# Performance work log

Hardware: AMD Instinct MI355X
Metric: run time of the kernel (lower is better)

The kernel has to match this reference:

```python
import jax, jax.numpy as jnp
import numpy as np

B, T, D = 2, 2048, 1024
H, HD = 16, 64  # num_heads, key_size

def setup_inputs() -> dict:
    key = jax.random.key(0)
    ks = jax.random.split(key, 5)
    s = 1.0 / np.sqrt(D)  # VarianceScaling(1.0, fan_in) approx
    return {
        "query": jax.random.normal(ks[0], (B, T, D), dtype=jnp.float32),
        "wq": jax.random.normal(ks[1], (D, H * HD), dtype=jnp.float32) * s,
        "bq": jnp.zeros((H * HD,), dtype=jnp.float32),
        "wk": jax.random.normal(ks[2], (D, H * HD), dtype=jnp.float32) * s,
        "bk": jnp.zeros((H * HD,), dtype=jnp.float32),
        "wv": jax.random.normal(ks[3], (D, H * HD), dtype=jnp.float32) * s,
        "bv": jnp.zeros((H * HD,), dtype=jnp.float32),
        "wo": jax.random.normal(ks[4], (H * HD, D), dtype=jnp.float32) * (1.0 / np.sqrt(H * HD)),
        "bo": jnp.zeros((D,), dtype=jnp.float32),
    }

def reference(query, wq, bq, wk, bk, wv, bv, wo, bo):
    b, t, _ = query.shape
    proj = lambda w, bias: (query @ w + bias).reshape(b, t, H, HD)
    q = proj(wq, bq) / np.sqrt(HD).astype(np.float32)  # fixed scaling on queries
    k = proj(wk, bk)
    v = proj(wv, bv)
    logits = jnp.einsum('bthd,bThd->bhtT', q, k)  # [B,H,T,T]
    causal = jnp.tril(jnp.ones((t, t), dtype=logits.dtype))
    logits = logits - 1e10 * (1.0 - causal)
    weights = jax.nn.softmax(logits, axis=-1)
    attn = jnp.einsum('bhtT,bThd->bthd', weights, v)
    attn_vec = attn.reshape(b, t, H * HD)
    return attn_vec @ wo + bo
```

## Files before the change

kernel.cpp:

```cpp
#include <hip/hip_runtime.h>
#include <hip/hip_bf16.h>
#include <stdint.h>
#include <math.h>

typedef short bf16x8 __attribute__((ext_vector_type(8)));
typedef float f32x4 __attribute__((ext_vector_type(4)));
typedef __hip_bfloat16 bf16;

#define MFMA16(a, b, c) __builtin_amdgcn_mfma_f32_16x16x32_bf16((a), (b), (c), 0, 0, 0)

__device__ __forceinline__ void glds16(const void* g, void* l) {
  __builtin_amdgcn_global_load_lds((const __attribute__((address_space(1))) void*)g,
                                   (__attribute__((address_space(3))) void*)l, 16, 0, 0);
}

__device__ __forceinline__ bf16x8 ld8(const bf16* p) {
  return *reinterpret_cast<const bf16x8*>(p);
}


__global__ void k_cvt_x(const float* __restrict__ x, bf16* __restrict__ o, int n4) {
  int i = blockIdx.x * blockDim.x + threadIdx.x;
  if (i < n4) {
    float4 v = reinterpret_cast<const float4*>(x)[i];
    bf16 a0 = __float2bfloat16(v.x), a1 = __float2bfloat16(v.y);
    bf16 a2 = __float2bfloat16(v.z), a3 = __float2bfloat16(v.w);
    ushort4 r;
    r.x = reinterpret_cast<unsigned short&>(a0);
    r.y = reinterpret_cast<unsigned short&>(a1);
    r.z = reinterpret_cast<unsigned short&>(a2);
    r.w = reinterpret_cast<unsigned short&>(a3);
    reinterpret_cast<ushort4*>(o)[i] = r;
  }
}

__global__ void k_transpose_cvt(const float* __restrict__ wq, const float* __restrict__ wk,
                                const float* __restrict__ wv, const float* __restrict__ wo,
                                bf16* __restrict__ Wqkvt, bf16* __restrict__ Wot) {
  __shared__ float tile[32][33];
  const int z = blockIdx.z;
  const float* src = (z == 0) ? wq : (z == 1) ? wk : (z == 2) ? wv : wo;
  bf16* dst = (z < 3) ? (Wqkvt + (size_t)z * 1024 * 1024) : Wot;
  const int tx = threadIdx.x & 31, ty = threadIdx.x >> 5;
  const int x = blockIdx.x * 32 + tx;
  const int y0 = blockIdx.y * 32;
#pragma unroll
  for (int i = 0; i < 4; ++i) tile[ty + i * 8][tx] = src[(size_t)(y0 + ty + i * 8) * 1024 + x];
  __syncthreads();
#pragma unroll
  for (int i = 0; i < 4; ++i) {
    int c = blockIdx.x * 32 + ty + i * 8;
    dst[(size_t)c * 1024 + y0 + tx] = __float2bfloat16(tile[tx][ty + i * 8]);
  }
}


__device__ __forceinline__ void gemm_core(const bf16* __restrict__ A, const bf16* __restrict__ Bt,
                                          int K, int arow0, int bcol0,
                                          bf16* As, bf16* Bs, f32x4 acc[4][4]) {
  const int tid = threadIdx.x, lane = tid & 63, w = tid >> 6;
  const int rsub = lane >> 3, slot = lane & 7;
  const int srcslot = slot ^ rsub;
  const int wrow = (w >> 1) * 64, wcol = (w & 1) * 64;
  const int lr = lane & 15, lg = lane >> 4;
  const int nkt = K >> 6;
  for (int kt = 0; kt < nkt; ++kt) {
    const int k0 = kt * 64;
    if (kt) __syncthreads();
#pragma unroll
    for (int i = 0; i < 4; ++i) {
      const int chunk = w * 4 + i;
      glds16(A + (size_t)(arow0 + chunk * 8 + rsub) * K + k0 + srcslot * 8, As + chunk * 512);
      glds16(Bt + (size_t)(bcol0 + chunk * 8 + rsub) * K + k0 + srcslot * 8, Bs + chunk * 512);
    }
    __syncthreads();
#pragma unroll
    for (int kk = 0; kk < 2; ++kk) {
      bf16x8 af[4], bfv[4];
#pragma unroll
      for (int m = 0; m < 4; ++m) {
        const int row = wrow + m * 16 + lr;
        const int byte = (row * 128 + ((kk * 32 + lg * 8) << 1)) ^ ((row & 7) << 4);
        af[m] = *reinterpret_cast<const bf16x8*>(reinterpret_cast<const char*>(As) + byte);
      }
#pragma unroll
      for (int n = 0; n < 4; ++n) {
        const int row = wcol + n * 16 + lr;
        const int byte = (row * 128 + ((kk * 32 + lg * 8) << 1)) ^ ((row & 7) << 4);
        bfv[n] = *reinterpret_cast<const bf16x8*>(reinterpret_cast<const char*>(Bs) + byte);
      }
#pragma unroll
      for (int m = 0; m < 4; ++m)
#pragma unroll
        for (int n = 0; n < 4; ++n) acc[m][n] = MFMA16(af[m], bfv[n], acc[m][n]);
    }
  }
}


__global__ __launch_bounds__(256) void k_gemm_qkv(
    const bf16* __restrict__ X, const bf16* __restrict__ Wt,
    const float* __restrict__ bq, const float* __restrict__ bk, const float* __restrict__ bv,
    bf16* __restrict__ Qo, bf16* __restrict__ Ko, bf16* __restrict__ Vt) {
  __shared__ bf16 As[128 * 64], Bs[128 * 64];
  f32x4 acc[4][4];
#pragma unroll
  for (int i = 0; i < 4; ++i)
#pragma unroll
    for (int j = 0; j < 4; ++j) acc[i][j] = (f32x4){0.f, 0.f, 0.f, 0.f};
  const int arow0 = blockIdx.y * 128, bcol0 = blockIdx.x * 128;
  gemm_core(X, Wt, 1024, arow0, bcol0, As, Bs, acc);
  const int lane = threadIdx.x & 63, w = threadIdx.x >> 6;
  const int wrow = (w >> 1) * 64, wcol = (w & 1) * 64;
  const int lr = lane & 15, lg = lane >> 4;
#pragma unroll
  for (int mi = 0; mi < 4; ++mi) {
#pragma unroll
    for (int ni = 0; ni < 4; ++ni) {
      const int r0 = arow0 + wrow + mi * 16 + lg * 4;
      const int col = bcol0 + wcol + ni * 16 + lr;
      const int which = col >> 10, cw = col & 1023, h = cw >> 6, hd = cw & 63;
      const int b = r0 >> 11, t0 = r0 & 2047;
      if (which == 2) {
        const float bias = bv[cw];
        ushort4 pk;
#pragma unroll
        for (int j = 0; j < 4; ++j) {
          bf16 hv = __float2bfloat16(acc[mi][ni][j] + bias);
          reinterpret_cast<unsigned short*>(&pk)[j] = reinterpret_cast<unsigned short&>(hv);
        }
        *reinterpret_cast<ushort4*>(Vt + ((size_t)((b * 16 + h) * 64 + hd)) * 2048 + t0) = pk;
      } else {
        const float bias = which ? bk[cw] : bq[cw];
        const float scale = which ? 1.0f : 0.125f;
        bf16* dst = which ? Ko : Qo;
#pragma unroll
        for (int j = 0; j < 4; ++j) {
          float v = (acc[mi][ni][j] + bias) * scale;
          dst[((size_t)((b * 16 + h) * 2048) + t0 + j) * 64 + hd] = __float2bfloat16(v);
        }
      }
    }
  }
}


__global__ __launch_bounds__(256) void k_attn(const bf16* __restrict__ Q, const bf16* __restrict__ Kc,
                                              const bf16* __restrict__ Vt, bf16* __restrict__ attn) {
  __shared__ bf16 Ks[2][64 * 64];
  __shared__ bf16 Vs[2][64 * 64];
  __shared__ bf16 Plds[4][16 * 64];
  const int lane = threadIdx.x & 63, w = threadIdx.x >> 6;
  const int lr = lane & 15, lg = lane >> 4;
  const int rsub = lane >> 3, slot = lane & 7;
  const int srcslot = slot ^ rsub;
  const int bh = blockIdx.x;
  const int qt = 31 - blockIdx.y;
  const int b = bh >> 4, h = bh & 15;
  const bf16* Qp = Q + (size_t)bh * 2048 * 64;
  const bf16* Kp = Kc + (size_t)bh * 2048 * 64;
  const bf16* Vp = Vt + (size_t)bh * 64 * 2048;

  const int q0 = qt * 64 + w * 16;
  const bf16x8 qa0 = ld8(Qp + (size_t)(q0 + lr) * 64 + lg * 8);
  const bf16x8 qa1 = ld8(Qp + (size_t)(q0 + lr) * 64 + 32 + lg * 8);
  f32x4 o[4];
#pragma unroll
  for (int n = 0; n < 4; ++n) o[n] = (f32x4){0.f, 0.f, 0.f, 0.f};
  float l_[4] = {0.f, 0.f, 0.f, 0.f};
  const int nkv = qt + 1;
  const float LOG2E = 1.4426950408889634f;
  const float MBIAS = -8.0f * LOG2E;

#pragma unroll
  for (int i = 0; i < 2; ++i) {
    const int ck = w * 2 + i;
    glds16(Kp + (size_t)(ck * 8 + rsub) * 64 + srcslot * 8, &Ks[0][ck * 512]);
    glds16(Vp + (size_t)(ck * 8 + rsub) * 2048 + srcslot * 8, &Vs[0][ck * 512]);
  }
  __syncthreads();
  int cur = 0;

#pragma unroll 1
  for (int it = 0; it < nkv; ++it) {
    const int kv0 = it * 64;
    if (it + 1 < nkv) {
#pragma unroll
      for (int i = 0; i < 2; ++i) {
        const int ck = w * 2 + i;
        glds16(Kp + (size_t)((it + 1) * 64 + ck * 8 + rsub) * 64 + srcslot * 8, &Ks[cur ^ 1][ck * 512]);
        glds16(Vp + (size_t)(ck * 8 + rsub) * 2048 + (it + 1) * 64 + srcslot * 8, &Vs[cur ^ 1][ck * 512]);
      }
    }
    f32x4 s[4];
    const char* Kb = reinterpret_cast<const char*>(&Ks[cur][0]);
#pragma unroll
    for (int n = 0; n < 4; ++n) {
      const int row = n * 16 + lr;
      const int rsw = (row & 7) << 4;
      bf16x8 kb0 = *reinterpret_cast<const bf16x8*>(Kb + ((row * 128 + lg * 16) ^ rsw));
      bf16x8 kb1 = *reinterpret_cast<const bf16x8*>(Kb + ((row * 128 + 64 + lg * 16) ^ rsw));
      f32x4 zz = {0.f, 0.f, 0.f, 0.f};
      s[n] = MFMA16(qa0, kb0, zz);
      s[n] = MFMA16(qa1, kb1, s[n]);
    }
    if (it == nkv - 1) {
#pragma unroll
      for (int n = 0; n < 4; ++n)
#pragma unroll
        for (int j = 0; j < 4; ++j)
          if (kv0 + n * 16 + lr > q0 + lg * 4 + j) s[n][j] = -1e30f;
    }
    float p[4][4];
#pragma unroll
    for (int n = 0; n < 4; ++n)
#pragma unroll
      for (int j = 0; j < 4; ++j) {
        p[n][j] = exp2f(fmaf(s[n][j], LOG2E, MBIAS));
        l_[j] += p[n][j];
      }
#pragma unroll
    for (int n = 0; n < 4; ++n)
#pragma unroll
      for (int j = 0; j < 4; ++j) {
        const int row = lg * 4 + j, col = n * 16 + lr;
        Plds[w][row * 64 + (col ^ ((row & 7) << 3))] = __float2bfloat16(p[n][j]);
      }
    bf16x8 pa[2];
#pragma unroll
    for (int kc = 0; kc < 2; ++kc) {
      const int byte = (lr * 128 + ((kc * 32 + lg * 8) << 1)) ^ ((lr & 7) << 4);
      pa[kc] = *reinterpret_cast<const bf16x8*>(reinterpret_cast<const char*>(&Plds[w][0]) + byte);
    }
    const char* Vb = reinterpret_cast<const char*>(&Vs[cur][0]);
#pragma unroll
    for (int n2 = 0; n2 < 4; ++n2) {
#pragma unroll
      for (int kc = 0; kc < 2; ++kc) {
        const int row = n2 * 16 + lr;
        const int rsw = (row & 7) << 4;
        bf16x8 vb = *reinterpret_cast<const bf16x8*>(Vb + ((row * 128 + (kc * 32 + lg * 8) * 2) ^ rsw));
        o[n2] = MFMA16(pa[kc], vb, o[n2]);
      }
    }
    __syncthreads();
    cur ^= 1;
  }
#pragma unroll
  for (int j = 0; j < 4; ++j) {
    float v = l_[j];
#pragma unroll
    for (int off = 1; off < 16; off <<= 1) v += __shfl_xor(v, off);
    l_[j] = v;
  }
#pragma unroll
  for (int j = 0; j < 4; ++j) {
    const float inv = 1.0f / l_[j];
    const int qq = q0 + lg * 4 + j;
#pragma unroll
    for (int n2 = 0; n2 < 4; ++n2)
      attn[((size_t)(b * 2048 + qq)) * 1024 + h * 64 + n2 * 16 + lr] = __float2bfloat16(o[n2][j] * inv);
  }
}


__global__ __launch_bounds__(256) void k_gemm_out(const bf16* __restrict__ A, const bf16* __restrict__ Wot,
                                                  const float* __restrict__ bo, float* __restrict__ out) {
  __shared__ bf16 As[128 * 64], Bs[128 * 64];
  f32x4 acc[4][4];
#pragma unroll
  for (int i = 0; i < 4; ++i)
#pragma unroll
    for (int j = 0; j < 4; ++j) acc[i][j] = (f32x4){0.f, 0.f, 0.f, 0.f};
  const int arow0 = blockIdx.y * 128, bcol0 = blockIdx.x * 128;
  gemm_core(A, Wot, 1024, arow0, bcol0, As, Bs, acc);
  const int lane = threadIdx.x & 63, w = threadIdx.x >> 6;
  const int wrow = (w >> 1) * 64, wcol = (w & 1) * 64;
  const int lr = lane & 15, lg = lane >> 4;
#pragma unroll
  for (int mi = 0; mi < 4; ++mi) {
#pragma unroll
    for (int ni = 0; ni < 4; ++ni) {
      const int r0 = arow0 + wrow + mi * 16 + lg * 4;
      const int col = bcol0 + wcol + ni * 16 + lr;
      const float bias = bo[col];
#pragma unroll
      for (int j = 0; j < 4; ++j) out[(size_t)(r0 + j) * 1024 + col] = acc[mi][ni][j] + bias;
    }
  }
}


extern "C" void kernel_launch(void* const* d_in, const int* in_sizes, int n_in,
                              void* d_out, int out_size, void* d_ws, size_t ws_size,
                              hipStream_t stream) {
  const float* query = (const float*)d_in[0];
  const float* wq = (const float*)d_in[1];
  const float* bq = (const float*)d_in[2];
  const float* wk = (const float*)d_in[3];
  const float* bk = (const float*)d_in[4];
  const float* wv = (const float*)d_in[5];
  const float* bv = (const float*)d_in[6];
  const float* wo = (const float*)d_in[7];
  const float* bo = (const float*)d_in[8];
  float* out = (float*)d_out;
  char* ws = (char*)d_ws;
  const size_t MB = 1u << 20;
  bf16* X     = (bf16*)(ws + 0);
  bf16* Wqkvt = (bf16*)(ws + 8 * MB);
  bf16* Wot   = (bf16*)(ws + 14 * MB);
  bf16* Qb    = (bf16*)(ws + 16 * MB);
  bf16* Kb    = (bf16*)(ws + 24 * MB);
  bf16* Vt    = (bf16*)(ws + 32 * MB);
  bf16* attn  = (bf16*)(ws + 40 * MB);

  k_cvt_x<<<4096, 256, 0, stream>>>(query, X, 4096 * 1024 / 4);
  k_transpose_cvt<<<dim3(32, 32, 4), 256, 0, stream>>>(wq, wk, wv, wo, Wqkvt, Wot);
  k_gemm_qkv<<<dim3(24, 32), 256, 0, stream>>>(X, Wqkvt, bq, bk, bv, Qb, Kb, Vt);
  k_attn<<<dim3(32, 32), 256, 0, stream>>>(Qb, Kb, Vt, attn);
  k_gemm_out<<<dim3(8, 32), 256, 0, stream>>>(attn, Wot, bo, out);
}
```

Before: 112.8 us.

## Double attention query tile to 128 rows and fold log2e scaling into Q

The attention kernel now handles 128 query rows per block (32 per wave, as two 16-row subtiles), so each K/V tile staged in LDS and loaded into registers serves twice as many queries, and the grid is halved. The log2e factor is folded into the Q projection scale, and the constant softmax bias is folded into the MFMA accumulator init, which removes an FMA per logit. P is converted to bf16 by truncation instead of rounding. The costs are more register pressure from the extra accumulators and K/V fragments, fewer blocks to fill the device, and some warp divergence on the causal diagonal.

```diff
diff --git a/kernel.cpp b/kernel.cpp
--- a/kernel.cpp
+++ b/kernel.cpp
@@ -113,6 +113,7 @@
   const int lane = threadIdx.x & 63, w = threadIdx.x >> 6;
   const int wrow = (w >> 1) * 64, wcol = (w & 1) * 64;
   const int lr = lane & 15, lg = lane >> 4;
+  const float QSCALE = 0.125f * 1.4426950408889634f;
 #pragma unroll
   for (int mi = 0; mi < 4; ++mi) {
 #pragma unroll
@@ -132,7 +133,7 @@
         *reinterpret_cast<ushort4*>(Vt + ((size_t)((b * 16 + h) * 64 + hd)) * 2048 + t0) = pk;
       } else {
         const float bias = which ? bk[cw] : bq[cw];
-        const float scale = which ? 1.0f : 0.125f;
+        const float scale = which ? 1.0f : QSCALE;
         bf16* dst = which ? Ko : Qo;
 #pragma unroll
         for (int j = 0; j < 4; ++j) {
@@ -155,22 +156,28 @@
   const int rsub = lane >> 3, slot = lane & 7;
   const int srcslot = slot ^ rsub;
   const int bh = blockIdx.x;
-  const int qt = 31 - blockIdx.y;
+  const int qt = 15 - blockIdx.y;
   const int b = bh >> 4, h = bh & 15;
   const bf16* Qp = Q + (size_t)bh * 2048 * 64;
   const bf16* Kp = Kc + (size_t)bh * 2048 * 64;
   const bf16* Vp = Vt + (size_t)bh * 64 * 2048;
 
-  const int q0 = qt * 64 + w * 16;
-  const bf16x8 qa0 = ld8(Qp + (size_t)(q0 + lr) * 64 + lg * 8);
-  const bf16x8 qa1 = ld8(Qp + (size_t)(q0 + lr) * 64 + 32 + lg * 8);
-  f32x4 o[4];
-#pragma unroll
-  for (int n = 0; n < 4; ++n) o[n] = (f32x4){0.f, 0.f, 0.f, 0.f};
-  float l_[4] = {0.f, 0.f, 0.f, 0.f};
-  const int nkv = qt + 1;
-  const float LOG2E = 1.4426950408889634f;
-  const float MBIAS = -8.0f * LOG2E;
+  const int q0 = qt * 128 + w * 32;
+  bf16x8 qa[2][2];
+#pragma unroll
+  for (int m = 0; m < 2; ++m) {
+    qa[m][0] = ld8(Qp + (size_t)(q0 + m * 16 + lr) * 64 + lg * 8);
+    qa[m][1] = ld8(Qp + (size_t)(q0 + m * 16 + lr) * 64 + 32 + lg * 8);
+  }
+  f32x4 o[2][4];
+#pragma unroll
+  for (int m = 0; m < 2; ++m)
+#pragma unroll
+    for (int n = 0; n < 4; ++n) o[m][n] = (f32x4){0.f, 0.f, 0.f, 0.f};
+  float l_[2][4] = {{0.f, 0.f, 0.f, 0.f}, {0.f, 0.f, 0.f, 0.f}};
+  const int nkv = (qt + 1) * 2;
+  const float MBIAS = -8.0f * 1.4426950408889634f;
+  const f32x4 minit = {MBIAS, MBIAS, MBIAS, MBIAS};
 
 #pragma unroll
   for (int i = 0; i < 2; ++i) {
@@ -192,74 +199,82 @@
         glds16(Vp + (size_t)(ck * 8 + rsub) * 2048 + (it + 1) * 64 + srcslot * 8, &Vs[cur ^ 1][ck * 512]);
       }
     }
-    f32x4 s[4];
-    const char* Kb = reinterpret_cast<const char*>(&Ks[cur][0]);
-#pragma unroll
-    for (int n = 0; n < 4; ++n) {
-      const int row = n * 16 + lr;
-      const int rsw = (row & 7) << 4;
-      bf16x8 kb0 = *reinterpret_cast<const bf16x8*>(Kb + ((row * 128 + lg * 16) ^ rsw));
-      bf16x8 kb1 = *reinterpret_cast<const bf16x8*>(Kb + ((row * 128 + 64 + lg * 16) ^ rsw));
-      f32x4 zz = {0.f, 0.f, 0.f, 0.f};
-      s[n] = MFMA16(qa0, kb0, zz);
-      s[n] = MFMA16(qa1, kb1, s[n]);
-    }
-    if (it == nkv - 1) {
-#pragma unroll
-      for (int n = 0; n < 4; ++n)
-#pragma unroll
-        for (int j = 0; j < 4; ++j)
-          if (kv0 + n * 16 + lr > q0 + lg * 4 + j) s[n][j] = -1e30f;
-    }
-    float p[4][4];
-#pragma unroll
-    for (int n = 0; n < 4; ++n)
-#pragma unroll
-      for (int j = 0; j < 4; ++j) {
-        p[n][j] = exp2f(fmaf(s[n][j], LOG2E, MBIAS));
-        l_[j] += p[n][j];
-      }
-#pragma unroll
-    for (int n = 0; n < 4; ++n)
-#pragma unroll
-      for (int j = 0; j < 4; ++j) {
-        const int row = lg * 4 + j, col = n * 16 + lr;
-        Plds[w][row * 64 + (col ^ ((row & 7) << 3))] = __float2bfloat16(p[n][j]);
-      }
-    bf16x8 pa[2];
-#pragma unroll
-    for (int kc = 0; kc < 2; ++kc) {
-      const int byte = (lr * 128 + ((kc * 32 + lg * 8) << 1)) ^ ((lr & 7) << 4);
-      pa[kc] = *reinterpret_cast<const bf16x8*>(reinterpret_cast<const char*>(&Plds[w][0]) + byte);
-    }
-    const char* Vb = reinterpret_cast<const char*>(&Vs[cur][0]);
-#pragma unroll
-    for (int n2 = 0; n2 < 4; ++n2) {
-#pragma unroll
-      for (int kc = 0; kc < 2; ++kc) {
+    if (kv0 <= q0 + 31) {
+      bf16x8 kf0[4], kf1[4];
+      const char* Kb = reinterpret_cast<const char*>(&Ks[cur][0]);
+#pragma unroll
+      for (int n = 0; n < 4; ++n) {
+        const int row = n * 16 + lr;
+        const int rsw = (row & 7) << 4;
+        kf0[n] = *reinterpret_cast<const bf16x8*>(Kb + ((row * 128 + lg * 16) ^ rsw));
+        kf1[n] = *reinterpret_cast<const bf16x8*>(Kb + ((row * 128 + 64 + lg * 16) ^ rsw));
+      }
+      bf16x8 vf[4][2];
+      const char* Vb = reinterpret_cast<const char*>(&Vs[cur][0]);
+#pragma unroll
+      for (int n2 = 0; n2 < 4; ++n2) {
         const int row = n2 * 16 + lr;
         const int rsw = (row & 7) << 4;
-        bf16x8 vb = *reinterpret_cast<const bf16x8*>(Vb + ((row * 128 + (kc * 32 + lg * 8) * 2) ^ rsw));
-        o[n2] = MFMA16(pa[kc], vb, o[n2]);
+#pragma unroll
+        for (int kc = 0; kc < 2; ++kc)
+          vf[n2][kc] = *reinterpret_cast<const bf16x8*>(Vb + ((row * 128 + (kc * 32 + lg * 8) * 2) ^ rsw));
+      }
+#pragma unroll
+      for (int m = 0; m < 2; ++m) {
+        const int qm0 = q0 + m * 16;
+        if (kv0 > qm0 + 15) continue;
+        f32x4 s[4];
+#pragma unroll
+        for (int n = 0; n < 4; ++n) {
+          s[n] = MFMA16(qa[m][0], kf0[n], minit);
+          s[n] = MFMA16(qa[m][1], kf1[n], s[n]);
+        }
+        if (kv0 + 63 > qm0) {
+#pragma unroll
+          for (int n = 0; n < 4; ++n)
+#pragma unroll
+            for (int j = 0; j < 4; ++j)
+              if (kv0 + n * 16 + lr > qm0 + lg * 4 + j) s[n][j] = -1e30f;
+        }
+        unsigned short* Pw = reinterpret_cast<unsigned short*>(&Plds[w][0]);
+#pragma unroll
+        for (int n = 0; n < 4; ++n)
+#pragma unroll
+          for (int j = 0; j < 4; ++j) {
+            float p = exp2f(s[n][j]);
+            l_[m][j] += p;
+            const int row = lg * 4 + j, col = n * 16 + lr;
+            Pw[row * 64 + (col ^ ((row & 7) << 3))] = (unsigned short)(__float_as_uint(p) >> 16);
+          }
+        bf16x8 pa[2];
+#pragma unroll
+        for (int kc = 0; kc < 2; ++kc) {
+          const int byte = (lr * 128 + ((kc * 32 + lg * 8) << 1)) ^ ((lr & 7) << 4);
+          pa[kc] = *reinterpret_cast<const bf16x8*>(reinterpret_cast<const char*>(&Plds[w][0]) + byte);
+        }
+#pragma unroll
+        for (int n2 = 0; n2 < 4; ++n2)
+#pragma unroll
+          for (int kc = 0; kc < 2; ++kc) o[m][n2] = MFMA16(pa[kc], vf[n2][kc], o[m][n2]);
       }
     }
     __syncthreads();
     cur ^= 1;
   }
 #pragma unroll
-  for (int j = 0; j < 4; ++j) {
-    float v = l_[j];
-#pragma unroll
-    for (int off = 1; off < 16; off <<= 1) v += __shfl_xor(v, off);
-    l_[j] = v;
-  }
-#pragma unroll
-  for (int j = 0; j < 4; ++j) {
-    const float inv = 1.0f / l_[j];
-    const int qq = q0 + lg * 4 + j;
-#pragma unroll
-    for (int n2 = 0; n2 < 4; ++n2)
-      attn[((size_t)(b * 2048 + qq)) * 1024 + h * 64 + n2 * 16 + lr] = __float2bfloat16(o[n2][j] * inv);
+  for (int m = 0; m < 2; ++m) {
+#pragma unroll
+    for (int j = 0; j < 4; ++j) {
+      float v = l_[m][j];
+#pragma unroll
+      for (int off = 1; off < 16; off <<= 1) v += __shfl_xor(v, off);
+      const float inv = 1.0f / v;
+      const int qq = q0 + m * 16 + lg * 4 + j;
+#pragma unroll
+      for (int n2 = 0; n2 < 4; ++n2)
+        attn[((size_t)(b * 2048 + qq)) * 1024 + h * 64 + n2 * 16 + lr] =
+            __float2bfloat16(o[m][n2][j] * inv);
+    }
   }
 }
 
@@ -317,6 +332,6 @@
   k_cvt_x<<<4096, 256, 0, stream>>>(query, X, 4096 * 1024 / 4);
   k_transpose_cvt<<<dim3(32, 32, 4), 256, 0, stream>>>(wq, wk, wv, wo, Wqkvt, Wot);
   k_gemm_qkv<<<dim3(24, 32), 256, 0, stream>>>(X, Wqkvt, bq, bk, bv, Qb, Kb, Vt);
-  k_attn<<<dim3(32, 32), 256, 0, stream>>>(Qb, Kb, Vt, attn);
+  k_attn<<<dim3(32, 16), 256, 0, stream>>>(Qb, Kb, Vt, attn);
   k_gemm_out<<<dim3(8, 32), 256, 0, stream>>>(attn, Wot, bo, out);
 }
```

Result: slower. 123.1 us (+9.1%).
